# Performance work log

Hardware: AMD Instinct MI355X
Metric: run time of the kernel (lower is better)

## Reference

```python
import jax, jax.numpy as jnp
import numpy as np

N_SUPPORT = 131072
NUM_CLASSES = 1024
D = 512
NUM_LEVELS = 3
LN_EPS = 1e-5


def setup_inputs() -> dict:
    key = jax.random.key(0)
    ks = jax.random.split(key, 10)
    s = 1.0 / np.sqrt(D)
    return {
        "support_features": jax.random.normal(ks[0], (N_SUPPORT, D), dtype=jnp.float32),
        "support_labels": jax.random.randint(ks[1], (N_SUPPORT,), 0, NUM_CLASSES, dtype=jnp.int32),
        "W1": jax.random.normal(ks[2], (NUM_LEVELS, D, D), dtype=jnp.float32) * s,
        "b1": jnp.zeros((NUM_LEVELS, D), dtype=jnp.float32),
        "ln_gamma": jnp.ones((NUM_LEVELS, D), dtype=jnp.float32),
        "ln_beta": jnp.zeros((NUM_LEVELS, D), dtype=jnp.float32),
        "W2": jax.random.normal(ks[3], (NUM_LEVELS, D, D), dtype=jnp.float32) * s,
        "b2": jnp.zeros((NUM_LEVELS, D), dtype=jnp.float32),
        "level_temperatures": jnp.ones((NUM_LEVELS,), dtype=jnp.float32),
    }


def _prototype_level(x, labels, w1, bb1, gamma, beta, w2, bb2, counts):
    # MLP: Linear -> LayerNorm -> ReLU -> (Dropout=identity, eval) -> Linear
    h = x @ w1 + bb1                                   # [N, D]
    mu = jnp.mean(h, axis=-1, keepdims=True)
    var = jnp.mean(jnp.square(h - mu), axis=-1, keepdims=True)
    h = (h - mu) * jax.lax.rsqrt(var + LN_EPS) * gamma + beta
    h = jax.nn.relu(h)
    h = h @ w2 + bb2                                   # [N, D]
    # per-class mean prototype (segment mean)
    sums = jax.ops.segment_sum(h, labels, num_segments=NUM_CLASSES)  # [C, D]
    return sums / counts


def reference(support_features, support_labels, W1, b1, ln_gamma, ln_beta, W2, b2, level_temperatures):
    labels = support_labels.astype(jnp.int32)
    counts = jax.ops.segment_sum(
        jnp.ones((support_features.shape[0],), dtype=support_features.dtype),
        labels, num_segments=NUM_CLASSES)
    counts = jnp.maximum(counts, 1.0)[:, None]         # [C, 1]

    level_protos = jax.vmap(
        lambda w1, bb1, g, bt, w2, bb2: _prototype_level(
            support_features, labels, w1, bb1, g, bt, w2, bb2, counts)
    )(W1, b1, ln_gamma, ln_beta, W2, b2)               # [L, C, D]

    level_weights = jax.nn.softmax(level_temperatures)  # [L]
    final_prototypes = jnp.einsum('l,lcd->cd', level_weights, level_protos)
    return final_prototypes
```

## Files before the change

### kernel.cpp

```cpp
#include <hip/hip_runtime.h>
#include <hip/hip_bf16.h>
#include <cstdint>

#define N_SUPPORT 131072
#define NUM_CLASSES 1024
#define DIM 512
#define LN_EPS 1e-5f

typedef __attribute__((ext_vector_type(8))) short bf16x8;
typedef __attribute__((ext_vector_type(4))) float f32x4;

__device__ __forceinline__ unsigned short f2bf(float f) {
  union { float f; uint32_t u; } c; c.f = f;
  uint32_t u = c.u;
  u += 0x7fffu + ((u >> 16) & 1u);
  return (unsigned short)(u >> 16);
}

__device__ __forceinline__ void gload16(const void* g, void* l) {
  __builtin_amdgcn_global_load_lds((const __attribute__((address_space(1))) void*)g,
                                   (__attribute__((address_space(3))) void*)l,
                                   16, 0, 0);
}

__global__ void k_hist(const int* __restrict__ labels, int* __restrict__ counts) {
  const int i = blockIdx.x * 256 + threadIdx.x;
  atomicAdd(&counts[labels[i]], 1);
}

__global__ void k_scan(const int* __restrict__ counts, int* __restrict__ offs,
                       float* __restrict__ invc) {
  __shared__ int tmp[1024];
  const int t = threadIdx.x;
  const int myc = counts[t];
  tmp[t] = myc;
  __syncthreads();
  for (int o = 1; o < 1024; o <<= 1) {
    int v = (t >= o) ? tmp[t - o] : 0;
    __syncthreads();
    tmp[t] += v;
    __syncthreads();
  }
  offs[t] = tmp[t] - myc;
  invc[t] = 1.0f / (float)max(myc, 1);
}

__global__ void k_scatter(const int* __restrict__ labels, const int* __restrict__ offs,
                          int* __restrict__ cursor, int* __restrict__ sorted) {
  const int i = blockIdx.x * 256 + threadIdx.x;
  const int c = labels[i];
  const int p = atomicAdd(&cursor[c], 1);
  sorted[offs[c] + p] = i;
}

__global__ void k_cast_sorted(const float* __restrict__ x, const int* __restrict__ sorted,
                              const int* __restrict__ labels,
                              unsigned short* __restrict__ xbt, int* __restrict__ scls) {
  const int tile = blockIdx.x;
  const int t = threadIdx.x;
  const int rr = t & 63, ksl = t >> 6;
  const int p = tile * 64 + rr;
  const int src = sorted[p];
  if (t < 64) scls[p] = labels[src];
  const float* xr = x + (size_t)src * DIM;
  #pragma unroll
  for (int kb = 0; kb < 4; ++kb) {
    const int ks = kb * 4 + ksl;
    float4 f[8];
    #pragma unroll
    for (int i = 0; i < 8; ++i) f[i] = *(const float4*)(xr + ks * 32 + i * 4);
    #pragma unroll
    for (int g = 0; g < 4; ++g) {
      uint4 o;
      o.x = (uint32_t)f2bf(f[g * 2].x) | ((uint32_t)f2bf(f[g * 2].y) << 16);
      o.y = (uint32_t)f2bf(f[g * 2].z) | ((uint32_t)f2bf(f[g * 2].w) << 16);
      o.z = (uint32_t)f2bf(f[g * 2 + 1].x) | ((uint32_t)f2bf(f[g * 2 + 1].y) << 16);
      o.w = (uint32_t)f2bf(f[g * 2 + 1].z) | ((uint32_t)f2bf(f[g * 2 + 1].w) << 16);
      *(uint4*)(xbt + ((size_t)(tile * 64 + ks * 4 + g)) * 512 + rr * 8) = o;
    }
  }
}

__global__ void k_prep_w1t(const float* __restrict__ w1, unsigned short* __restrict__ w1t) {
  const int i = blockIdx.x * 256 + threadIdx.x;
  const int l = i >> 15;
  const int ks = (i >> 11) & 15;
  const int g = (i >> 9) & 3;
  const int n = i & 511;
  const float* src = w1 + ((size_t)l * 512 + ks * 32 + g * 8) * 512 + n;
  unsigned short v[8];
  #pragma unroll
  for (int e = 0; e < 8; ++e) v[e] = f2bf(src[(size_t)e * 512]);
  uint4 o;
  o.x = (uint32_t)v[0] | ((uint32_t)v[1] << 16);
  o.y = (uint32_t)v[2] | ((uint32_t)v[3] << 16);
  o.z = (uint32_t)v[4] | ((uint32_t)v[5] << 16);
  o.w = (uint32_t)v[6] | ((uint32_t)v[7] << 16);
  *(uint4*)(w1t + (size_t)i * 8) = o;
}

__global__ __launch_bounds__(256, 2) void k_gemm1lnred(
    const unsigned short* __restrict__ XbT, const unsigned short* __restrict__ W1T,
    const float* __restrict__ b1, const float* __restrict__ gamma, const float* __restrict__ beta,
    const int* __restrict__ scls_g, float* __restrict__ M)
{
  __shared__ unsigned short sX[4 * 64 * 8];
  __shared__ unsigned short sW[4 * 512 * 8];
  __shared__ float wsum[4][64];
  __shared__ float wsq[4][64];
  __shared__ float smean[64];
  __shared__ float srstd[64];
  __shared__ int scls[64];
  __shared__ int run_start[65];
  __shared__ int run_cls[64];
  __shared__ int nruns_s;

  const int t = threadIdx.x;
  const int wv = t >> 6;
  const int lane = t & 63;
  const int lr = lane & 15;
  const int lq = lane >> 4;
  const int l = blockIdx.x;
  const int tile = blockIdx.y;
  const int row0 = tile * 64;

  const unsigned short* xsrc = XbT + (size_t)tile * 32768;
  const unsigned short* wsrc = W1T + (size_t)l * 262144;

  f32x4 acc[4][8];
  #pragma unroll
  for (int i = 0; i < 4; ++i)
    #pragma unroll
    for (int j = 0; j < 8; ++j) acc[i][j] = (f32x4){0.f, 0.f, 0.f, 0.f};

  if (t < 64) scls[t] = scls_g[row0 + t];

  unsigned short* sXw = sX + wv * 512;
  for (int ks = 0; ks < 16; ++ks) {
    gload16(xsrc + (size_t)ks * 2048 + t * 8, sXw);
    #pragma unroll
    for (int i = 0; i < 8; ++i)
      gload16(wsrc + (size_t)ks * 16384 + (i * 256 + t) * 8, sW + (i * 256 + wv * 64) * 8);
    __syncthreads();

    bf16x8 a[4], b[8];
    #pragma unroll
    for (int rf = 0; rf < 4; ++rf)
      a[rf] = *(const bf16x8*)(sX + (lq * 64 + rf * 16 + lr) * 8);
    #pragma unroll
    for (int cf = 0; cf < 8; ++cf)
      b[cf] = *(const bf16x8*)(sW + (lq * 512 + wv * 128 + cf * 16 + lr) * 8);

    #pragma unroll
    for (int rf = 0; rf < 4; ++rf)
      #pragma unroll
      for (int cf = 0; cf < 8; ++cf)
        acc[rf][cf] = __builtin_amdgcn_mfma_f32_16x16x32_bf16(a[rf], b[cf], acc[rf][cf], 0, 0, 0);
    __syncthreads();
  }

  float b1v[8], gv[8], bv[8];
  #pragma unroll
  for (int cf = 0; cf < 8; ++cf) {
    const int col = wv * 128 + cf * 16 + lr;
    b1v[cf] = b1[l * 512 + col];
    gv[cf] = gamma[l * 512 + col];
    bv[cf] = beta[l * 512 + col];
  }
  #pragma unroll
  for (int rf = 0; rf < 4; ++rf)
    #pragma unroll
    for (int cf = 0; cf < 8; ++cf)
      #pragma unroll
      for (int j = 0; j < 4; ++j) acc[rf][cf][j] += b1v[cf];

  #pragma unroll
  for (int rf = 0; rf < 4; ++rf) {
    #pragma unroll
    for (int j = 0; j < 4; ++j) {
      float s = 0.f, q = 0.f;
      #pragma unroll
      for (int cf = 0; cf < 8; ++cf) { float v = acc[rf][cf][j]; s += v; q += v * v; }
      #pragma unroll
      for (int m = 8; m >= 1; m >>= 1) { s += __shfl_xor(s, m, 16); q += __shfl_xor(q, m, 16); }
      if (lr == 0) { const int row = rf * 16 + lq * 4 + j; wsum[wv][row] = s; wsq[wv][row] = q; }
    }
  }
  __syncthreads();
  if (t < 64) {
    const float s = wsum[0][t] + wsum[1][t] + wsum[2][t] + wsum[3][t];
    const float q = wsq[0][t] + wsq[1][t] + wsq[2][t] + wsq[3][t];
    const float mean = s * (1.0f / 512.0f);
    const float var = q * (1.0f / 512.0f) - mean * mean;
    smean[t] = mean;
    srstd[t] = rsqrtf(var + LN_EPS);
  }
  if (t == 0) {
    int n = 0;
    run_start[0] = 0;
    run_cls[0] = scls[0];
    for (int r = 1; r < 64; ++r) {
      if (scls[r] != scls[r - 1]) { ++n; run_start[n] = r; run_cls[n] = scls[r]; }
    }
    nruns_s = n + 1;
    run_start[n + 1] = 64;
  }
  __syncthreads();

  #pragma unroll
  for (int rf = 0; rf < 4; ++rf) {
    #pragma unroll
    for (int j = 0; j < 4; ++j) {
      const int row = rf * 16 + lq * 4 + j;
      const float mean = smean[row], rs = srstd[row];
      #pragma unroll
      for (int cf = 0; cf < 8; ++cf) {
        float v = (acc[rf][cf][j] - mean) * rs * gv[cf] + bv[cf];
        acc[rf][cf][j] = fmaxf(v, 0.f);
      }
    }
  }

  const int nruns = nruns_s;
  float* Ml = M + (size_t)l * NUM_CLASSES * DIM;
  for (int r = 0; r < nruns; ++r) {
    const int rs = run_start[r], re = run_start[r + 1];
    const int cls = run_cls[r];
    float p[8];
    #pragma unroll
    for (int cf = 0; cf < 8; ++cf) p[cf] = 0.f;
    #pragma unroll
    for (int rf = 0; rf < 4; ++rf) {
      #pragma unroll
      for (int j = 0; j < 4; ++j) {
        const int row = rf * 16 + lq * 4 + j;
        if (row >= rs && row < re) {
          #pragma unroll
          for (int cf = 0; cf < 8; ++cf) p[cf] += acc[rf][cf][j];
        }
      }
    }
    #pragma unroll
    for (int cf = 0; cf < 8; ++cf) {
      p[cf] += __shfl_xor(p[cf], 16);
      p[cf] += __shfl_xor(p[cf], 32);
    }
    if (lq == 0) {
      #pragma unroll
      for (int cf = 0; cf < 8; ++cf)
        atomicAdd(&Ml[(size_t)cls * DIM + wv * 128 + cf * 16 + lr], p[cf]);
    }
  }
}

__global__ void k_final(const float* __restrict__ M, const float* __restrict__ W2,
                        const float* __restrict__ b2, const float* __restrict__ temps,
                        const float* __restrict__ invc, float* __restrict__ out)
{
  __shared__ float sA[64][17];
  __shared__ float sB[16][65];
  const int t = threadIdx.x;
  const int tx = t & 15, ty = t >> 4;
  const int bcol = blockIdx.x * 64;
  const int brow = blockIdx.y * 64;
  const int l = blockIdx.z;

  const float t0 = temps[0], t1 = temps[1], t2 = temps[2];
  const float mx = fmaxf(t0, fmaxf(t1, t2));
  const float e0 = expf(t0 - mx), e1 = expf(t1 - mx), e2 = expf(t2 - mx);
  const float inv = 1.f / (e0 + e1 + e2);
  const float w[3] = {e0 * inv, e1 * inv, e2 * inv};
  const float wl = w[l];

  float acc[4][4] = {};
  for (int k0 = 0; k0 < 512; k0 += 16) {
    __syncthreads();
    #pragma unroll
    for (int i = 0; i < 4; ++i) {
      const int e = i * 256 + t;
      const int r = e >> 4, k = e & 15;
      sA[r][k] = M[((size_t)l * 1024 + brow + r) * 512 + k0 + k] * (wl * invc[brow + r]);
    }
    #pragma unroll
    for (int i = 0; i < 4; ++i) {
      const int e = i * 256 + t;
      const int r = e >> 6, nn = e & 63;
      sB[r][nn] = W2[((size_t)l * 512 + k0 + r) * 512 + bcol + nn];
    }
    __syncthreads();
    #pragma unroll
    for (int kk = 0; kk < 16; ++kk) {
      float a[4], b[4];
      #pragma unroll
      for (int i = 0; i < 4; ++i) a[i] = sA[ty * 4 + i][kk];
      #pragma unroll
      for (int j = 0; j < 4; ++j) b[j] = sB[kk][tx * 4 + j];
      #pragma unroll
      for (int i = 0; i < 4; ++i)
        #pragma unroll
        for (int j = 0; j < 4; ++j) acc[i][j] += a[i] * b[j];
    }
  }
  #pragma unroll
  for (int j = 0; j < 4; ++j) {
    const int col = bcol + tx * 4 + j;
    const float bias = (l == 0)
        ? (w[0] * b2[col] + w[1] * b2[512 + col] + w[2] * b2[1024 + col]) : 0.f;
    #pragma unroll
    for (int i = 0; i < 4; ++i)
      atomicAdd(&out[(size_t)(brow + ty * 4 + i) * 512 + col], acc[i][j] + bias);
  }
}

extern "C" void kernel_launch(void* const* d_in, const int* in_sizes, int n_in,
                              void* d_out, int out_size, void* d_ws, size_t ws_size,
                              hipStream_t stream)
{
  const float* X = (const float*)d_in[0];
  const int* labels = (const int*)d_in[1];
  const float* W1 = (const float*)d_in[2];
  const float* b1 = (const float*)d_in[3];
  const float* gamma = (const float*)d_in[4];
  const float* beta = (const float*)d_in[5];
  const float* W2 = (const float*)d_in[6];
  const float* b2 = (const float*)d_in[7];
  const float* temps = (const float*)d_in[8];
  float* out = (float*)d_out;

  char* ws = (char*)d_ws;
  size_t off = 0;
  auto alloc = [&](size_t bytes) -> char* {
    char* p = ws + off;
    off += (bytes + 255) & ~(size_t)255;
    return p;
  };
  unsigned short* XbT = (unsigned short*)alloc((size_t)N_SUPPORT * DIM * 2);
  unsigned short* W1T = (unsigned short*)alloc((size_t)3 * 512 * 512 * 2);
  float* M = (float*)alloc((size_t)3 * 1024 * 512 * 4);
  int* counts = (int*)alloc(2048 * 4);
  int* cursor = counts + 1024;
  int* offs = (int*)alloc(1024 * 4);
  float* invc = (float*)alloc(1024 * 4);
  int* sorted = (int*)alloc((size_t)N_SUPPORT * 4);
  int* scls = (int*)alloc((size_t)N_SUPPORT * 4);

  hipMemsetAsync(counts, 0, 2048 * 4, stream);
  hipMemsetAsync(M, 0, (size_t)3 * 1024 * 512 * 4, stream);
  hipMemsetAsync(out, 0, (size_t)NUM_CLASSES * DIM * 4, stream);
  k_hist<<<512, 256, 0, stream>>>(labels, counts);
  k_scan<<<1, 1024, 0, stream>>>(counts, offs, invc);
  k_scatter<<<512, 256, 0, stream>>>(labels, offs, cursor, sorted);
  k_cast_sorted<<<2048, 256, 0, stream>>>(X, sorted, labels, XbT, scls);
  k_prep_w1t<<<384, 256, 0, stream>>>(W1, W1T);
  k_gemm1lnred<<<dim3(3, 2048), 256, 0, stream>>>(XbT, W1T, b1, gamma, beta, scls, M);
  k_final<<<dim3(8, 16, 3), 256, 0, stream>>>(M, W2, b2, temps, invc, out);
}
```

Before: 856.0 us.

## Load GEMM1 operands directly to registers with double buffering; fold levels in final GEMM

The main GEMM kernel stops staging X and W1 tiles through LDS with barriers. Each wave now loads its MFMA fragments straight from global memory into registers, double-buffered across k-steps, so no __syncthreads are needed. W1 fragments are shared by all row tiles and may hit in cache, but every wave now issues redundant global loads and register pressure rises. The final kernel loops over the three levels inside one block and writes the output directly, removing the output memset and atomics at the cost of a third as many blocks.

```diff
diff --git a/kernel.cpp b/kernel.cpp
--- a/kernel.cpp
+++ b/kernel.cpp
@@ -15,12 +15,6 @@
   uint32_t u = c.u;
   u += 0x7fffu + ((u >> 16) & 1u);
   return (unsigned short)(u >> 16);
-}
-
-__device__ __forceinline__ void gload16(const void* g, void* l) {
-  __builtin_amdgcn_global_load_lds((const __attribute__((address_space(1))) void*)g,
-                                   (__attribute__((address_space(3))) void*)l,
-                                   16, 0, 0);
 }
 
 __global__ void k_hist(const int* __restrict__ labels, int* __restrict__ counts) {
@@ -104,8 +98,6 @@
     const float* __restrict__ b1, const float* __restrict__ gamma, const float* __restrict__ beta,
     const int* __restrict__ scls_g, float* __restrict__ M)
 {
-  __shared__ unsigned short sX[4 * 64 * 8];
-  __shared__ unsigned short sW[4 * 512 * 8];
   __shared__ float wsum[4][64];
   __shared__ float wsq[4][64];
   __shared__ float smean[64];
@@ -124,8 +116,10 @@
   const int tile = blockIdx.y;
   const int row0 = tile * 64;
 
-  const unsigned short* xsrc = XbT + (size_t)tile * 32768;
-  const unsigned short* wsrc = W1T + (size_t)l * 262144;
+  if (t < 64) scls[t] = scls_g[row0 + t];
+
+  const unsigned short* pa = XbT + (size_t)tile * 32768 + lq * 512 + lr * 8;
+  const unsigned short* pb = W1T + (size_t)l * 262144 + lq * 4096 + (wv * 128 + lr) * 8;
 
   f32x4 acc[4][8];
   #pragma unroll
@@ -133,30 +127,34 @@
     #pragma unroll
     for (int j = 0; j < 8; ++j) acc[i][j] = (f32x4){0.f, 0.f, 0.f, 0.f};
 
-  if (t < 64) scls[t] = scls_g[row0 + t];
-
-  unsigned short* sXw = sX + wv * 512;
-  for (int ks = 0; ks < 16; ++ks) {
-    gload16(xsrc + (size_t)ks * 2048 + t * 8, sXw);
-    #pragma unroll
-    for (int i = 0; i < 8; ++i)
-      gload16(wsrc + (size_t)ks * 16384 + (i * 256 + t) * 8, sW + (i * 256 + wv * 64) * 8);
-    __syncthreads();
-
-    bf16x8 a[4], b[8];
+  bf16x8 a0[4], b0[8], a1[4], b1v8[8];
+  #pragma unroll
+  for (int rf = 0; rf < 4; ++rf) a0[rf] = *(const bf16x8*)(pa + rf * 128);
+  #pragma unroll
+  for (int cf = 0; cf < 8; ++cf) b0[cf] = *(const bf16x8*)(pb + cf * 128);
+
+  #pragma unroll
+  for (int ks = 0; ks < 16; ks += 2) {
+    #pragma unroll
+    for (int rf = 0; rf < 4; ++rf) a1[rf] = *(const bf16x8*)(pa + (ks + 1) * 2048 + rf * 128);
+    #pragma unroll
+    for (int cf = 0; cf < 8; ++cf) b1v8[cf] = *(const bf16x8*)(pb + (ks + 1) * 16384 + cf * 128);
     #pragma unroll
     for (int rf = 0; rf < 4; ++rf)
-      a[rf] = *(const bf16x8*)(sX + (lq * 64 + rf * 16 + lr) * 8);
-    #pragma unroll
-    for (int cf = 0; cf < 8; ++cf)
-      b[cf] = *(const bf16x8*)(sW + (lq * 512 + wv * 128 + cf * 16 + lr) * 8);
-
+      #pragma unroll
+      for (int cf = 0; cf < 8; ++cf)
+        acc[rf][cf] = __builtin_amdgcn_mfma_f32_16x16x32_bf16(a0[rf], b0[cf], acc[rf][cf], 0, 0, 0);
+    if (ks + 2 < 16) {
+      #pragma unroll
+      for (int rf = 0; rf < 4; ++rf) a0[rf] = *(const bf16x8*)(pa + (ks + 2) * 2048 + rf * 128);
+      #pragma unroll
+      for (int cf = 0; cf < 8; ++cf) b0[cf] = *(const bf16x8*)(pb + (ks + 2) * 16384 + cf * 128);
+    }
     #pragma unroll
     for (int rf = 0; rf < 4; ++rf)
       #pragma unroll
       for (int cf = 0; cf < 8; ++cf)
-        acc[rf][cf] = __builtin_amdgcn_mfma_f32_16x16x32_bf16(a[rf], b[cf], acc[rf][cf], 0, 0, 0);
-    __syncthreads();
+        acc[rf][cf] = __builtin_amdgcn_mfma_f32_16x16x32_bf16(a1[rf], b1v8[cf], acc[rf][cf], 0, 0, 0);
   }
 
   float b1v[8], gv[8], bv[8];
@@ -263,52 +261,51 @@
   const int tx = t & 15, ty = t >> 4;
   const int bcol = blockIdx.x * 64;
   const int brow = blockIdx.y * 64;
-  const int l = blockIdx.z;
 
   const float t0 = temps[0], t1 = temps[1], t2 = temps[2];
   const float mx = fmaxf(t0, fmaxf(t1, t2));
   const float e0 = expf(t0 - mx), e1 = expf(t1 - mx), e2 = expf(t2 - mx);
   const float inv = 1.f / (e0 + e1 + e2);
   const float w[3] = {e0 * inv, e1 * inv, e2 * inv};
-  const float wl = w[l];
 
   float acc[4][4] = {};
-  for (int k0 = 0; k0 < 512; k0 += 16) {
-    __syncthreads();
-    #pragma unroll
-    for (int i = 0; i < 4; ++i) {
-      const int e = i * 256 + t;
-      const int r = e >> 4, k = e & 15;
-      sA[r][k] = M[((size_t)l * 1024 + brow + r) * 512 + k0 + k] * (wl * invc[brow + r]);
-    }
-    #pragma unroll
-    for (int i = 0; i < 4; ++i) {
-      const int e = i * 256 + t;
-      const int r = e >> 6, nn = e & 63;
-      sB[r][nn] = W2[((size_t)l * 512 + k0 + r) * 512 + bcol + nn];
-    }
-    __syncthreads();
-    #pragma unroll
-    for (int kk = 0; kk < 16; ++kk) {
-      float a[4], b[4];
-      #pragma unroll
-      for (int i = 0; i < 4; ++i) a[i] = sA[ty * 4 + i][kk];
-      #pragma unroll
-      for (int j = 0; j < 4; ++j) b[j] = sB[kk][tx * 4 + j];
-      #pragma unroll
-      for (int i = 0; i < 4; ++i)
+  for (int l = 0; l < 3; ++l) {
+    for (int k0 = 0; k0 < 512; k0 += 16) {
+      __syncthreads();
+      #pragma unroll
+      for (int i = 0; i < 4; ++i) {
+        const int e = i * 256 + t;
+        const int r = e >> 4, k = e & 15;
+        sA[r][k] = M[((size_t)l * 1024 + brow + r) * 512 + k0 + k] * (w[l] * invc[brow + r]);
+      }
+      #pragma unroll
+      for (int i = 0; i < 4; ++i) {
+        const int e = i * 256 + t;
+        const int r = e >> 6, nn = e & 63;
+        sB[r][nn] = W2[((size_t)l * 512 + k0 + r) * 512 + bcol + nn];
+      }
+      __syncthreads();
+      #pragma unroll
+      for (int kk = 0; kk < 16; ++kk) {
+        float a[4], b[4];
         #pragma unroll
-        for (int j = 0; j < 4; ++j) acc[i][j] += a[i] * b[j];
+        for (int i = 0; i < 4; ++i) a[i] = sA[ty * 4 + i][kk];
+        #pragma unroll
+        for (int j = 0; j < 4; ++j) b[j] = sB[kk][tx * 4 + j];
+        #pragma unroll
+        for (int i = 0; i < 4; ++i)
+          #pragma unroll
+          for (int j = 0; j < 4; ++j) acc[i][j] += a[i] * b[j];
+      }
     }
   }
   #pragma unroll
   for (int j = 0; j < 4; ++j) {
     const int col = bcol + tx * 4 + j;
-    const float bias = (l == 0)
-        ? (w[0] * b2[col] + w[1] * b2[512 + col] + w[2] * b2[1024 + col]) : 0.f;
+    const float bias = w[0] * b2[col] + w[1] * b2[512 + col] + w[2] * b2[1024 + col];
     #pragma unroll
     for (int i = 0; i < 4; ++i)
-      atomicAdd(&out[(size_t)(brow + ty * 4 + i) * 512 + col], acc[i][j] + bias);
+      out[(size_t)(brow + ty * 4 + i) * 512 + col] = acc[i][j] + bias;
   }
 }
 
@@ -346,12 +343,11 @@
 
   hipMemsetAsync(counts, 0, 2048 * 4, stream);
   hipMemsetAsync(M, 0, (size_t)3 * 1024 * 512 * 4, stream);
-  hipMemsetAsync(out, 0, (size_t)NUM_CLASSES * DIM * 4, stream);
   k_hist<<<512, 256, 0, stream>>>(labels, counts);
   k_scan<<<1, 1024, 0, stream>>>(counts, offs, invc);
   k_scatter<<<512, 256, 0, stream>>>(labels, offs, cursor, sorted);
   k_cast_sorted<<<2048, 256, 0, stream>>>(X, sorted, labels, XbT, scls);
   k_prep_w1t<<<384, 256, 0, stream>>>(W1, W1T);
   k_gemm1lnred<<<dim3(3, 2048), 256, 0, stream>>>(XbT, W1T, b1, gamma, beta, scls, M);
-  k_final<<<dim3(8, 16, 3), 256, 0, stream>>>(M, W2, b2, temps, invc, out);
-}
+  k_final<<<dim3(8, 16), 256, 0, stream>>>(M, W2, b2, temps, invc, out);
+}
```

Result: slower. 939.0 us (+9.7%).
